# Performance work log

Hardware: AMD Instinct MI355X
Metric: run time of the kernel (lower is better)

Reference implementation:

```python
import jax, jax.numpy as jnp
import numpy as np

K = 3
STRIDE = 2
SQRT_D = 4  # in_d_capsules = 16 -> 4x4 matrix pose
LN_EPS = 1e-5


def _unfold(x, k, s):
    # x: [B, N, H, W, A] -> [B, N, k, k, Hout, Wout, A] (matches torch unfold+permute)
    B, N, H, W, A = x.shape
    Hout = (H - k) // s + 1
    Wout = (W - k) // s + 1
    hi = jnp.arange(Hout) * s
    wi = jnp.arange(Wout) * s
    x1 = x[:, :, hi[:, None] + jnp.arange(k)[None, :]]            # [B,N,Hout,k,W,A]
    x2 = x1[:, :, :, :, wi[:, None] + jnp.arange(k)[None, :]]     # [B,N,Hout,k,Wout,k,A]
    return jnp.transpose(x2, (0, 1, 3, 5, 2, 4, 6))               # [B,N,k,k,Hout,Wout,A]


def setup_inputs() -> dict:
    key = jax.random.key(0)
    k1, k2, k3 = jax.random.split(key, 3)
    B, N_in, H, W, D_in = 32, 32, 32, 32, 16
    N_out, D_out = 32, 16
    Hout = (H - K) // STRIDE + 1
    Wout = (W - K) // STRIDE + 1
    w_const = np.sqrt(N_out / (SQRT_D * N_in * K * K)).astype(np.float32)
    return {
        "input": jax.random.normal(k1, (B, N_in, H, W, D_in), dtype=jnp.float32),
        "next_capsule_value": jax.random.normal(k2, (B, N_out, Hout, Wout, D_out), dtype=jnp.float32),
        "w": w_const * jax.random.normal(k3, (K, K, N_in, SQRT_D, SQRT_D, N_out), dtype=jnp.float32),
        "gamma": jnp.ones((D_out,), dtype=jnp.float32),
        "beta": jnp.zeros((D_out,), dtype=jnp.float32),
        "num_iter": 1,
    }


def reference(input, next_capsule_value, w, gamma, beta, num_iter):
    out_d = SQRT_D * SQRT_D
    scale = 1.0 / np.sqrt(out_d).astype(np.float32)
    inp = _unfold(input, K, STRIDE)                                # [B,N,k,k,h,w,A]
    B, N, _, _, h, wd, A = inp.shape
    _inp = inp.reshape(B, N, K, K, h, wd, SQRT_D, SQRT_D)          # bnklhwax
    M = next_capsule_value.shape[1]
    ncv = next_capsule_value.reshape(B, M, h, wd, SQRT_D, SQRT_D)  # bmhwad
    # query-key routing logits
    qk = jnp.einsum('bnklhwax,klnxdm,bmhwad->bnklmhw', _inp, w, ncv) * scale
    qk = jax.nn.softmax(qk, axis=4)
    qk = qk / (jnp.sum(qk, axis=4, keepdims=True) + 1e-10)
    # value aggregation
    out = jnp.einsum('bnklmhw,bnklhwax,klnxdm->bmhwad', qk, _inp, w)
    out = out.reshape(B, M, h, wd, out_d)
    # dropout p=0 -> identity; LayerNorm over capsule dim
    mu = jnp.mean(out, axis=-1, keepdims=True)
    var = jnp.var(out, axis=-1, keepdims=True)
    out = (out - mu) / jnp.sqrt(var + LN_EPS) * gamma + beta
    return out
```

## Files before the change

kernel.cpp:

```cpp
#include <hip/hip_runtime.h>

#define HOUT 15
#define WOUT 15

#define ASG __attribute__((address_space(1)))
#define ASL __attribute__((address_space(3)))

typedef float v2 __attribute__((ext_vector_type(2)));

__global__ __launch_bounds__(256, 2) void caps_part(
    const float* __restrict__ input,
    const float* __restrict__ ncv,
    const float* __restrict__ wt,
    float* __restrict__ part0,
    float* __restrict__ part1)
{
    __shared__ float lw[2][4608];

    const int tid   = threadIdx.x;
    const int grp   = tid >> 5;
    const int lane  = tid & 31;
    const int wv    = tid >> 6;
    const int wlane = tid & 63;

    const int pos = blockIdx.x * 8 + grp;
    const int b   = pos / (HOUT * WOUT);
    const int hw  = pos % (HOUT * WOUT);
    const int h   = hw / WOUT;
    const int wo  = hw % WOUT;

    const int s  = blockIdx.y;
    const int n0 = s * 16;

    auto stage = [&](int n, int buf) {
        for (int t = wv; t < 18; t += 4) {
            const int c = t >> 1, half = t & 1;
            const float* src = wt + c * 16384 + n * 512 + half * 256 + wlane * 4;
            float* dst = &lw[buf][c * 512 + half * 256];
            __builtin_amdgcn_global_load_lds((const ASG void*)src, (ASL void*)dst,
                                             16, 0, 0);
        }
    };

    stage(n0, 0);

    const float* ncv_p = ncv + ((((size_t)b * 32 + lane) * HOUT + h) * WOUT + wo) * 16;
    v2 cv2[8];
#pragma unroll
    for (int j = 0; j < 8; ++j) cv2[j] = *(const v2*)(ncv_p + j * 2);

    v2 acc2[8];
#pragma unroll
    for (int j = 0; j < 8; ++j) acc2[j] = (v2){0.0f, 0.0f};

    const int h0 = h * 2, w0 = wo * 2;

    __syncthreads();

    for (int i = 0; i < 16; ++i) {
        const int n = n0 + i;
        if (i + 1 < 16) stage(n + 1, (i + 1) & 1);

        const float* wbuf = lw[i & 1];
        const float* ipn  = input + ((((size_t)b * 32 + n) * 32 + h0) * 32 + w0) * 16;

#pragma unroll
        for (int k = 0; k < 3; ++k) {
#pragma unroll
            for (int l = 0; l < 3; ++l) {
                const int kl = k * 3 + l;
                const float* ip = ipn + (k * 32 + l) * 16;
                float av[16];
#pragma unroll
                for (int j = 0; j < 16; j += 4) {
                    float4 t = *(const float4*)(ip + j);
                    av[j] = t.x; av[j + 1] = t.y; av[j + 2] = t.z; av[j + 3] = t.w;
                }

                const float* wp = wbuf + kl * 512 + lane;

                v2 u2[8];
#pragma unroll
                for (int j = 0; j < 8; ++j) u2[j] = (v2){0.0f, 0.0f};
#pragma unroll
                for (int x = 0; x < 4; ++x) {
                    float wd0 = wp[(x * 4 + 0) * 32];
                    float wd1 = wp[(x * 4 + 1) * 32];
                    float wd2 = wp[(x * 4 + 2) * 32];
                    float wd3 = wp[(x * 4 + 3) * 32];
                    v2 wlo = {wd0, wd1};
                    v2 whi = {wd2, wd3};
#pragma unroll
                    for (int a = 0; a < 4; ++a) {
                        v2 sp = {av[a * 4 + x], av[a * 4 + x]};
                        u2[a * 2 + 0] = __builtin_elementwise_fma(sp, wlo, u2[a * 2 + 0]);
                        u2[a * 2 + 1] = __builtin_elementwise_fma(sp, whi, u2[a * 2 + 1]);
                    }
                }

                v2 d0 = {0.f, 0.f}, d1 = {0.f, 0.f};
#pragma unroll
                for (int j = 0; j < 4; ++j) {
                    d0 = __builtin_elementwise_fma(u2[j],     cv2[j],     d0);
                    d1 = __builtin_elementwise_fma(u2[j + 4], cv2[j + 4], d1);
                }
                v2 dd = d0 + d1;
                float logit = (dd.x + dd.y) * 0.25f;

                float e = __expf(logit);
                float sum = e;
#pragma unroll
                for (int o = 16; o > 0; o >>= 1)
                    sum += __shfl_xor(sum, o, 32);
                float p = e * __builtin_amdgcn_rcpf(sum);
                v2 p2 = {p, p};

#pragma unroll
                for (int j = 0; j < 8; ++j)
                    acc2[j] = __builtin_elementwise_fma(p2, u2[j], acc2[j]);
            }
        }

        if (i < 15) __syncthreads();
    }

    float* op = (s == 0 ? part0 : part1)
              + ((((size_t)b * 32 + lane) * HOUT + h) * WOUT + wo) * 16;
#pragma unroll
    for (int j = 0; j < 4; ++j) {
        float4 r;
        r.x = acc2[2 * j].x;     r.y = acc2[2 * j].y;
        r.z = acc2[2 * j + 1].x; r.w = acc2[2 * j + 1].y;
        *(float4*)(op + j * 4) = r;
    }
}

__global__ __launch_bounds__(256) void caps_ln(
    const float* __restrict__ part1,
    const float* __restrict__ gamma,
    const float* __restrict__ beta,
    float* __restrict__ out)
{
    const size_t t = (size_t)blockIdx.x * 256 + threadIdx.x;
    const float* p0 = out   + t * 16;
    const float* p1 = part1 + t * 16;

    float a[16];
#pragma unroll
    for (int j = 0; j < 16; j += 4) {
        float4 x = *(const float4*)(p0 + j);
        float4 y = *(const float4*)(p1 + j);
        a[j] = x.x + y.x; a[j+1] = x.y + y.y; a[j+2] = x.z + y.z; a[j+3] = x.w + y.w;
    }

    float mu = 0.0f;
#pragma unroll
    for (int j = 0; j < 16; ++j) mu += a[j];
    mu *= 0.0625f;
    float var = 0.0f;
#pragma unroll
    for (int j = 0; j < 16; ++j) { float d = a[j] - mu; var = fmaf(d, d, var); }
    var *= 0.0625f;
    float rstd = __builtin_amdgcn_rsqf(var + 1e-5f);

    float* op = out + t * 16;
#pragma unroll
    for (int j = 0; j < 16; j += 4) {
        float4 g  = *(const float4*)(gamma + j);
        float4 be = *(const float4*)(beta + j);
        float4 r;
        r.x = (a[j + 0] - mu) * rstd * g.x + be.x;
        r.y = (a[j + 1] - mu) * rstd * g.y + be.y;
        r.z = (a[j + 2] - mu) * rstd * g.z + be.z;
        r.w = (a[j + 3] - mu) * rstd * g.w + be.w;
        *(float4*)(op + j) = r;
    }
}

extern "C" void kernel_launch(void* const* d_in, const int* in_sizes, int n_in,
                              void* d_out, int out_size, void* d_ws, size_t ws_size,
                              hipStream_t stream) {
    const float* input = (const float*)d_in[0];
    const float* ncv   = (const float*)d_in[1];
    const float* wt    = (const float*)d_in[2];
    const float* gamma = (const float*)d_in[3];
    const float* beta  = (const float*)d_in[4];
    float* out  = (float*)d_out;
    float* ws   = (float*)d_ws;

    caps_part<<<dim3(900, 2), dim3(256), 0, stream>>>(input, ncv, wt, out, ws);
    caps_ln<<<dim3(900), dim3(256), 0, stream>>>(ws, gamma, beta, out);
}
```

Baseline: 379.8 us.

## Fuse LayerNorm into main kernel, pre-transpose weights, read W via global float4

```diff
diff --git a/kernel.cpp b/kernel.cpp
--- a/kernel.cpp
+++ b/kernel.cpp
@@ -3,46 +3,43 @@
 #define HOUT 15
 #define WOUT 15
 
-#define ASG __attribute__((address_space(1)))
-#define ASL __attribute__((address_space(3)))
-
 typedef float v2 __attribute__((ext_vector_type(2)));
 
-__global__ __launch_bounds__(256, 2) void caps_part(
+#define DPP_ADDF(x, ctrl) \
+    ((x) + __builtin_bit_cast(float, __builtin_amdgcn_update_dpp( \
+        0, __builtin_bit_cast(int, (x)), (ctrl), 0xF, 0xF, true)))
+
+__global__ __launch_bounds__(256) void prep_w(const float* __restrict__ wt,
+                                              float* __restrict__ w2)
+{
+    const int t  = blockIdx.x * 256 + threadIdx.x;
+    const int d  = t & 3;
+    const int m  = (t >> 2) & 31;
+    const int x  = (t >> 7) & 3;
+    const int r  = t >> 9;
+    const int kl = r % 9;
+    const int n  = r / 9;
+    w2[t] = wt[((((kl * 32 + n) * 4 + x) * 4 + d) * 32) + m];
+}
+
+__global__ __launch_bounds__(128, 4) void caps_fused(
     const float* __restrict__ input,
     const float* __restrict__ ncv,
-    const float* __restrict__ wt,
-    float* __restrict__ part0,
-    float* __restrict__ part1)
+    const float* __restrict__ w2,
+    const float* __restrict__ gamma,
+    const float* __restrict__ beta,
+    float* __restrict__ out)
 {
-    __shared__ float lw[2][4608];
+    const int tid  = threadIdx.x;
+    const int grp  = tid >> 5;
+    const int lane = tid & 31;
 
-    const int tid   = threadIdx.x;
-    const int grp   = tid >> 5;
-    const int lane  = tid & 31;
-    const int wv    = tid >> 6;
-    const int wlane = tid & 63;
-
-    const int pos = blockIdx.x * 8 + grp;
+    const int pos = blockIdx.x * 4 + grp;
     const int b   = pos / (HOUT * WOUT);
     const int hw  = pos % (HOUT * WOUT);
     const int h   = hw / WOUT;
     const int wo  = hw % WOUT;
-
-    const int s  = blockIdx.y;
-    const int n0 = s * 16;
-
-    auto stage = [&](int n, int buf) {
-        for (int t = wv; t < 18; t += 4) {
-            const int c = t >> 1, half = t & 1;
-            const float* src = wt + c * 16384 + n * 512 + half * 256 + wlane * 4;
-            float* dst = &lw[buf][c * 512 + half * 256];
-            __builtin_amdgcn_global_load_lds((const ASG void*)src, (ASL void*)dst,
-                                             16, 0, 0);
-        }
-    };
-
-    stage(n0, 0);
+    const int h0  = h * 2, w0 = wo * 2;
 
     const float* ncv_p = ncv + ((((size_t)b * 32 + lane) * HOUT + h) * WOUT + wo) * 16;
     v2 cv2[8];
@@ -53,127 +50,98 @@
 #pragma unroll
     for (int j = 0; j < 8; ++j) acc2[j] = (v2){0.0f, 0.0f};
 
-    const int h0 = h * 2, w0 = wo * 2;
+    const float* ip0 = input + ((((size_t)b * 32) * 32 + h0) * 32 + w0) * 16;
+    const float* wp0 = w2 + lane * 4;
 
-    __syncthreads();
-
-    for (int i = 0; i < 16; ++i) {
-        const int n = n0 + i;
-        if (i + 1 < 16) stage(n + 1, (i + 1) & 1);
-
-        const float* wbuf = lw[i & 1];
-        const float* ipn  = input + ((((size_t)b * 32 + n) * 32 + h0) * 32 + w0) * 16;
+    for (int n = 0; n < 32; ++n) {
+        const float* ipn = ip0 + (size_t)n * 16384;
+        const float* wpn = wp0 + (size_t)n * 4608;
 
 #pragma unroll
-        for (int k = 0; k < 3; ++k) {
+        for (int kl = 0; kl < 9; ++kl) {
+            const int k = kl / 3, l = kl % 3;
+            const float* ip = ipn + (k * 32 + l) * 16;
+
+            float av[16];
 #pragma unroll
-            for (int l = 0; l < 3; ++l) {
-                const int kl = k * 3 + l;
-                const float* ip = ipn + (k * 32 + l) * 16;
-                float av[16];
+            for (int j = 0; j < 16; j += 4) {
+                float4 t4 = *(const float4*)(ip + j);
+                av[j] = t4.x; av[j + 1] = t4.y; av[j + 2] = t4.z; av[j + 3] = t4.w;
+            }
+
+            const float* wp = wpn + kl * 512;
+            float4 wx[4];
 #pragma unroll
-                for (int j = 0; j < 16; j += 4) {
-                    float4 t = *(const float4*)(ip + j);
-                    av[j] = t.x; av[j + 1] = t.y; av[j + 2] = t.z; av[j + 3] = t.w;
-                }
+            for (int x = 0; x < 4; ++x) wx[x] = *(const float4*)(wp + x * 128);
 
-                const float* wp = wbuf + kl * 512 + lane;
-
-                v2 u2[8];
+            v2 u2[8];
 #pragma unroll
-                for (int j = 0; j < 8; ++j) u2[j] = (v2){0.0f, 0.0f};
+            for (int x = 0; x < 4; ++x) {
+                v2 wlo = {wx[x].x, wx[x].y};
+                v2 whi = {wx[x].z, wx[x].w};
 #pragma unroll
-                for (int x = 0; x < 4; ++x) {
-                    float wd0 = wp[(x * 4 + 0) * 32];
-                    float wd1 = wp[(x * 4 + 1) * 32];
-                    float wd2 = wp[(x * 4 + 2) * 32];
-                    float wd3 = wp[(x * 4 + 3) * 32];
-                    v2 wlo = {wd0, wd1};
-                    v2 whi = {wd2, wd3};
-#pragma unroll
-                    for (int a = 0; a < 4; ++a) {
-                        v2 sp = {av[a * 4 + x], av[a * 4 + x]};
-                        u2[a * 2 + 0] = __builtin_elementwise_fma(sp, wlo, u2[a * 2 + 0]);
+                for (int a = 0; a < 4; ++a) {
+                    v2 sp = {av[a * 4 + x], av[a * 4 + x]};
+                    if (x == 0) {
+                        u2[a * 2]     = sp * wlo;
+                        u2[a * 2 + 1] = sp * whi;
+                    } else {
+                        u2[a * 2]     = __builtin_elementwise_fma(sp, wlo, u2[a * 2]);
                         u2[a * 2 + 1] = __builtin_elementwise_fma(sp, whi, u2[a * 2 + 1]);
                     }
                 }
+            }
 
-                v2 d0 = {0.f, 0.f}, d1 = {0.f, 0.f};
+            v2 d0 = {0.f, 0.f}, d1 = {0.f, 0.f};
 #pragma unroll
-                for (int j = 0; j < 4; ++j) {
-                    d0 = __builtin_elementwise_fma(u2[j],     cv2[j],     d0);
-                    d1 = __builtin_elementwise_fma(u2[j + 4], cv2[j + 4], d1);
-                }
-                v2 dd = d0 + d1;
-                float logit = (dd.x + dd.y) * 0.25f;
+            for (int j = 0; j < 4; ++j) {
+                d0 = __builtin_elementwise_fma(u2[j],     cv2[j],     d0);
+                d1 = __builtin_elementwise_fma(u2[j + 4], cv2[j + 4], d1);
+            }
+            v2 dd = d0 + d1;
+            float e = __builtin_exp2f((dd.x + dd.y) * 0.36067376022224085f);
 
-                float e = __expf(logit);
-                float sum = e;
+            float s = e;
+            s = DPP_ADDF(s, 0xB1);
+            s = DPP_ADDF(s, 0x4E);
+            s = DPP_ADDF(s, 0x141);
+            s = DPP_ADDF(s, 0x140);
+            s += __builtin_bit_cast(float,
+                  __builtin_amdgcn_ds_swizzle(__builtin_bit_cast(int, s), 0x401F));
+
+            float p = e * __builtin_amdgcn_rcpf(s);
+            v2 p2 = {p, p};
 #pragma unroll
-                for (int o = 16; o > 0; o >>= 1)
-                    sum += __shfl_xor(sum, o, 32);
-                float p = e * __builtin_amdgcn_rcpf(sum);
-                v2 p2 = {p, p};
-
-#pragma unroll
-                for (int j = 0; j < 8; ++j)
-                    acc2[j] = __builtin_elementwise_fma(p2, u2[j], acc2[j]);
-            }
+            for (int j = 0; j < 8; ++j)
+                acc2[j] = __builtin_elementwise_fma(p2, u2[j], acc2[j]);
         }
-
-        if (i < 15) __syncthreads();
     }
 
-    float* op = (s == 0 ? part0 : part1)
-              + ((((size_t)b * 32 + lane) * HOUT + h) * WOUT + wo) * 16;
+    v2 sv = acc2[0];
+#pragma unroll
+    for (int j = 1; j < 8; ++j) sv = sv + acc2[j];
+    float mu = (sv.x + sv.y) * 0.0625f;
+    v2 mv = {mu, mu};
+    v2 vv = {0.f, 0.f};
+#pragma unroll
+    for (int j = 0; j < 8; ++j) {
+        v2 dlt = acc2[j] - mv;
+        vv = __builtin_elementwise_fma(dlt, dlt, vv);
+    }
+    float var  = (vv.x + vv.y) * 0.0625f;
+    float rstd = __builtin_amdgcn_rsqf(var + 1e-5f);
+
+    float* op = out + ((((size_t)b * 32 + lane) * HOUT + h) * WOUT + wo) * 16;
 #pragma unroll
     for (int j = 0; j < 4; ++j) {
+        float4 g  = *(const float4*)(gamma + j * 4);
+        float4 be = *(const float4*)(beta  + j * 4);
         float4 r;
-        r.x = acc2[2 * j].x;     r.y = acc2[2 * j].y;
-        r.z = acc2[2 * j + 1].x; r.w = acc2[2 * j + 1].y;
+        r.x = (acc2[2 * j].x     - mu) * rstd * g.x + be.x;
+        r.y = (acc2[2 * j].y     - mu) * rstd * g.y + be.y;
+        r.z = (acc2[2 * j + 1].x - mu) * rstd * g.z + be.z;
+        r.w = (acc2[2 * j + 1].y - mu) * rstd * g.w + be.w;
         *(float4*)(op + j * 4) = r;
-    }
-}
-
-__global__ __launch_bounds__(256) void caps_ln(
-    const float* __restrict__ part1,
-    const float* __restrict__ gamma,
-    const float* __restrict__ beta,
-    float* __restrict__ out)
-{
-    const size_t t = (size_t)blockIdx.x * 256 + threadIdx.x;
-    const float* p0 = out   + t * 16;
-    const float* p1 = part1 + t * 16;
-
-    float a[16];
-#pragma unroll
-    for (int j = 0; j < 16; j += 4) {
-        float4 x = *(const float4*)(p0 + j);
-        float4 y = *(const float4*)(p1 + j);
-        a[j] = x.x + y.x; a[j+1] = x.y + y.y; a[j+2] = x.z + y.z; a[j+3] = x.w + y.w;
-    }
-
-    float mu = 0.0f;
-#pragma unroll
-    for (int j = 0; j < 16; ++j) mu += a[j];
-    mu *= 0.0625f;
-    float var = 0.0f;
-#pragma unroll
-    for (int j = 0; j < 16; ++j) { float d = a[j] - mu; var = fmaf(d, d, var); }
-    var *= 0.0625f;
-    float rstd = __builtin_amdgcn_rsqf(var + 1e-5f);
-
-    float* op = out + t * 16;
-#pragma unroll
-    for (int j = 0; j < 16; j += 4) {
-        float4 g  = *(const float4*)(gamma + j);
-        float4 be = *(const float4*)(beta + j);
-        float4 r;
-        r.x = (a[j + 0] - mu) * rstd * g.x + be.x;
-        r.y = (a[j + 1] - mu) * rstd * g.y + be.y;
-        r.z = (a[j + 2] - mu) * rstd * g.z + be.z;
-        r.w = (a[j + 3] - mu) * rstd * g.w + be.w;
-        *(float4*)(op + j) = r;
     }
 }
 
@@ -185,9 +153,9 @@
     const float* wt    = (const float*)d_in[2];
     const float* gamma = (const float*)d_in[3];
     const float* beta  = (const float*)d_in[4];
-    float* out  = (float*)d_out;
-    float* ws   = (float*)d_ws;
+    float* out = (float*)d_out;
+    float* w2  = (float*)d_ws;
 
-    caps_part<<<dim3(900, 2), dim3(256), 0, stream>>>(input, ncv, wt, out, ws);
-    caps_ln<<<dim3(900), dim3(256), 0, stream>>>(ws, gamma, beta, out);
+    prep_w<<<dim3(576), dim3(256), 0, stream>>>(wt, w2);
+    caps_fused<<<dim3(1800), dim3(128), 0, stream>>>(input, ncv, w2, gamma, beta, out);
 }
```

Result: no change. 386.6 us (+1.8%).
